# Optimization experiments

Hardware: AMD Instinct MI355X
Metric: run time of the kernel (lower is better)

## Reference

```python
import jax, jax.numpy as jnp
import numpy as np

MARGIN = 0.3
N, D = 4096, 512
NUM_CLASSES = 64

def setup_inputs() -> dict:
    key = jax.random.key(0)
    k1, k2, k3 = jax.random.split(key, 3)
    src_feat = jax.random.normal(k1, (N, D), dtype=jnp.float32)
    tgt_feat = jax.random.normal(k2, (N, D), dtype=jnp.float32)
    labels = jax.random.randint(k3, (N,), 0, NUM_CLASSES, dtype=jnp.int64)
    return {"src_feat": src_feat, "tgt_feat": tgt_feat, "labels": labels}

def reference(src_feat, tgt_feat, labels):
    # squared Euclidean distance matrix [n, n]
    e1 = jnp.sum(src_feat * src_feat, axis=1, keepdims=True)   # [n,1]
    e2 = jnp.sum(tgt_feat * tgt_feat, axis=1, keepdims=True).T  # [1,n]
    dist = e1 + e2 - 2.0 * (src_feat @ tgt_feat.T)
    dist = jnp.maximum(dist, 0.0)  # matches dist_mat[dist_mat < 0] = 0
    # same-label mask [n, n]
    mask = labels[:, None] == labels[None, :]
    # hard positive: max dist among same-label cols; hard negative: min among others
    dist_ap = jnp.max(jnp.where(mask, dist, -jnp.inf), axis=1)  # [n]
    dist_an = jnp.min(jnp.where(mask, jnp.inf, dist), axis=1)   # [n]
    # MarginRankingLoss with target y = 1: mean(relu(-(an - ap) + margin))
    loss = jnp.mean(jax.nn.relu(dist_ap - dist_an + MARGIN))
    return loss
```

## Files before the change

kernel.cpp:

```cpp
#include <hip/hip_runtime.h>
#include <hip/hip_bf16.h>
#include <stdint.h>

#define N_PTS 4096
#define DIM 512
#define MARGIN_F 0.3f
#define POS_INF_BITS 0x7f800000

typedef short bf16x8 __attribute__((ext_vector_type(8)));
typedef float f32x4 __attribute__((ext_vector_type(4)));

__device__ __forceinline__ unsigned short f2bf(float f) {
    unsigned int b = __float_as_uint(f);
    b += 0x7FFF + ((b >> 16) & 1);
    return (unsigned short)(b >> 16);
}

__device__ __forceinline__ void async16(const unsigned short* g, unsigned short* l) {
    __builtin_amdgcn_global_load_lds(
        (const __attribute__((address_space(1))) unsigned int*)g,
        (__attribute__((address_space(3))) unsigned int*)l,
        16, 0, 0);
}

#define RAW_BARRIER()  asm volatile("s_barrier" ::: "memory")
#define WAIT_VM12()    asm volatile("s_waitcnt vmcnt(12)" ::: "memory")
#define WAIT_VM6()     asm volatile("s_waitcnt vmcnt(6)" ::: "memory")
#define WAIT_VM0()     asm volatile("s_waitcnt vmcnt(0)" ::: "memory")

__global__ __launch_bounds__(256) void prep_kernel(
    const float* __restrict__ src, const float* __restrict__ tgt,
    unsigned short* __restrict__ src_bf, unsigned short* __restrict__ tgt_bf,
    float* __restrict__ e1, float* __restrict__ e2,
    float* __restrict__ out)
{
    const int row  = blockIdx.x * 4 + (threadIdx.x >> 6);
    const int lane = threadIdx.x & 63;

    if (blockIdx.x == 0 && threadIdx.x == 0) out[0] = 0.0f;

    const float4* s4 = (const float4*)(src + (size_t)row * DIM);
    const float4* t4 = (const float4*)(tgt + (size_t)row * DIM);
    float4 a0 = s4[lane], a1 = s4[lane + 64];
    float4 b0 = t4[lane], b1 = t4[lane + 64];

    ushort4 u;
    ushort4* so = (ushort4*)(src_bf + (size_t)row * DIM);
    ushort4* to = (ushort4*)(tgt_bf + (size_t)row * DIM);
    u.x = f2bf(a0.x); u.y = f2bf(a0.y); u.z = f2bf(a0.z); u.w = f2bf(a0.w); so[lane] = u;
    u.x = f2bf(a1.x); u.y = f2bf(a1.y); u.z = f2bf(a1.z); u.w = f2bf(a1.w); so[lane + 64] = u;
    u.x = f2bf(b0.x); u.y = f2bf(b0.y); u.z = f2bf(b0.z); u.w = f2bf(b0.w); to[lane] = u;
    u.x = f2bf(b1.x); u.y = f2bf(b1.y); u.z = f2bf(b1.z); u.w = f2bf(b1.w); to[lane + 64] = u;

    float s1 = a0.x*a0.x + a0.y*a0.y + a0.z*a0.z + a0.w*a0.w
             + a1.x*a1.x + a1.y*a1.y + a1.z*a1.z + a1.w*a1.w;
    float s2 = b0.x*b0.x + b0.y*b0.y + b0.z*b0.z + b0.w*b0.w
             + b1.x*b1.x + b1.y*b1.y + b1.z*b1.z + b1.w*b1.w;
    for (int off = 32; off; off >>= 1) {
        s1 += __shfl_down(s1, off);
        s2 += __shfl_down(s2, off);
    }
    if (lane == 0) {
        e1[row] = s1;
        e2[row] = s2;
    }
}

#define BM 128
#define BN 256
#define BK 32
#define NSTEP (DIM / BK)
#define NPART 64

__global__ __launch_bounds__(256, 2) void dist_kernel(
    const unsigned short* __restrict__ src_bf,
    const unsigned short* __restrict__ tgt_bf,
    const float* __restrict__ e1, const float* __restrict__ e2,
    const int* __restrict__ labels,
    float* __restrict__ ap_part, float* __restrict__ an_part)
{
    __shared__ unsigned short As[3][BM * BK];
    __shared__ unsigned short Bs[3][BN * BK];
    __shared__ int   li[BM];
    __shared__ int   lj[BN];
    __shared__ float e1s[BM];
    __shared__ float e2s[BN];

    const int i0 = blockIdx.y * BM;
    const int j0 = blockIdx.x * BN;
    const int t = threadIdx.x;
    const int lane = t & 63;
    const int wave = t >> 6;

    lj[t] = labels[j0 + t];
    e2s[t] = e2[j0 + t];
    if (t < BM) { li[t] = labels[i0 + t]; e1s[t] = e1[i0 + t]; }

    const int srow = t >> 2;
    const int scol = ((t & 3) ^ ((srow >> 1) & 3)) * 8;
    const unsigned short* gA0 = src_bf + (size_t)(i0 + srow) * DIM + scol;
    const unsigned short* gA1 = src_bf + (size_t)(i0 + 64 + srow) * DIM + scol;
    const unsigned short* gB0 = tgt_bf + (size_t)(j0 + srow) * DIM + scol;
    const unsigned short* gB1 = tgt_bf + (size_t)(j0 + 64 + srow) * DIM + scol;
    const unsigned short* gB2 = tgt_bf + (size_t)(j0 + 128 + srow) * DIM + scol;
    const unsigned short* gB3 = tgt_bf + (size_t)(j0 + 192 + srow) * DIM + scol;
    const int aOff0 = wave * 512;
    const int aOff1 = 2048 + wave * 512;
    const int bOff0 = wave * 512;
    const int bOff1 = 2048 + wave * 512;
    const int bOff2 = 4096 + wave * 512;
    const int bOff3 = 6144 + wave * 512;

    const int wn = wave * 64;
    const int fr = lane & 15;
    const int quad = lane >> 4;
    const int fkey = (fr >> 1) & 3;
    const int cp = (quad ^ fkey) * 8;

    f32x4 acc[8][4];
    #pragma unroll
    for (int a = 0; a < 8; a++)
        #pragma unroll
        for (int b = 0; b < 4; b++)
            acc[a][b] = (f32x4){0.f, 0.f, 0.f, 0.f};

    #pragma unroll
    for (int p = 0; p < 2; p++) {
        const int kk = p * BK;
        async16(gA0 + kk, &As[p][0] + aOff0);
        async16(gA1 + kk, &As[p][0] + aOff1);
        async16(gB0 + kk, &Bs[p][0] + bOff0);
        async16(gB1 + kk, &Bs[p][0] + bOff1);
        async16(gB2 + kk, &Bs[p][0] + bOff2);
        async16(gB3 + kk, &Bs[p][0] + bOff3);
    }

    #pragma unroll
    for (int s = 0; s < NSTEP; s++) {
        if (s + 2 < NSTEP) {
            const int kk = (s + 2) * BK;
            const int nb = (s + 2) % 3;
            async16(gA0 + kk, &As[nb][0] + aOff0);
            async16(gA1 + kk, &As[nb][0] + aOff1);
            async16(gB0 + kk, &Bs[nb][0] + bOff0);
            async16(gB1 + kk, &Bs[nb][0] + bOff1);
            async16(gB2 + kk, &Bs[nb][0] + bOff2);
            async16(gB3 + kk, &Bs[nb][0] + bOff3);
            WAIT_VM12();
        } else if (s + 2 == NSTEP) {
            WAIT_VM6();
        } else {
            WAIT_VM0();
        }
        RAW_BARRIER();

        const unsigned short* aa = &As[s % 3][0];
        const unsigned short* bb = &Bs[s % 3][0];
        bf16x8 af[8], bf[4];
        #pragma unroll
        for (int x = 0; x < 8; x++)
            af[x] = *(const bf16x8*)&aa[(x * 16 + fr) * BK + cp];
        #pragma unroll
        for (int x = 0; x < 4; x++)
            bf[x] = *(const bf16x8*)&bb[(wn + x * 16 + fr) * BK + cp];
        #pragma unroll
        for (int tm = 0; tm < 8; tm++)
            #pragma unroll
            for (int tn = 0; tn < 4; tn++)
                acc[tm][tn] = __builtin_amdgcn_mfma_f32_16x16x32_bf16(
                    af[tm], bf[tn], acc[tm][tn], 0, 0, 0);

        if (s + 1 < NSTEP)
            RAW_BARRIER();
    }

    const float INF = __int_as_float(POS_INF_BITS);
    const int pcol = blockIdx.x * 4 + wave;
    #pragma unroll
    for (int tm = 0; tm < 8; tm++) {
        #pragma unroll
        for (int r = 0; r < 4; r++) {
            const int rl = tm * 16 + quad * 4 + r;
            const float e1v = e1s[rl];
            const int   liv = li[rl];
            float apv = 0.0f;
            float anv = INF;
            #pragma unroll
            for (int tn = 0; tn < 4; tn++) {
                const int cl = wn + tn * 16 + fr;
                float d = e1v + e2s[cl] - 2.0f * acc[tm][tn][r];
                d = fmaxf(d, 0.0f);
                if (liv == lj[cl]) apv = fmaxf(apv, d);
                else               anv = fminf(anv, d);
            }
            #pragma unroll
            for (int off = 1; off < 16; off <<= 1) {
                apv = fmaxf(apv, __shfl_xor(apv, off));
                anv = fminf(anv, __shfl_xor(anv, off));
            }
            if (fr == 0) {
                ap_part[(size_t)(i0 + rl) * NPART + pcol] = apv;
                an_part[(size_t)(i0 + rl) * NPART + pcol] = anv;
            }
        }
    }
}

__global__ __launch_bounds__(128) void loss_kernel(
    const float* __restrict__ ap_part, const float* __restrict__ an_part,
    float* __restrict__ out)
{
    const int row = blockIdx.x * 128 + threadIdx.x;
    const float4* a4 = (const float4*)(ap_part + (size_t)row * NPART);
    const float4* n4 = (const float4*)(an_part + (size_t)row * NPART);
    float apv = 0.0f;
    float anv = __int_as_float(POS_INF_BITS);
    #pragma unroll
    for (int i = 0; i < NPART / 4; i++) {
        float4 a = a4[i], n = n4[i];
        apv = fmaxf(apv, fmaxf(fmaxf(a.x, a.y), fmaxf(a.z, a.w)));
        anv = fminf(anv, fminf(fminf(n.x, n.y), fminf(n.z, n.w)));
    }
    float s = fmaxf(apv - anv + MARGIN_F, 0.0f);
    for (int off = 32; off; off >>= 1) s += __shfl_down(s, off);
    __shared__ float red[2];
    if ((threadIdx.x & 63) == 0) red[threadIdx.x >> 6] = s;
    __syncthreads();
    if (threadIdx.x == 0)
        atomicAdd(out, (red[0] + red[1]) / (float)N_PTS);
}

extern "C" void kernel_launch(void* const* d_in, const int* in_sizes, int n_in,
                              void* d_out, int out_size, void* d_ws, size_t ws_size,
                              hipStream_t stream) {
    const float* src   = (const float*)d_in[0];
    const float* tgt   = (const float*)d_in[1];
    const int* labels  = (const int*)d_in[2];

    char* ws = (char*)d_ws;
    const size_t featB = (size_t)N_PTS * DIM * sizeof(unsigned short);
    unsigned short* src_bf = (unsigned short*)ws;
    unsigned short* tgt_bf = (unsigned short*)(ws + featB);
    float* e1 = (float*)(ws + 2 * featB);
    float* e2 = e1 + N_PTS;
    float* ap_part = e2 + N_PTS;
    float* an_part = ap_part + (size_t)N_PTS * NPART;

    prep_kernel<<<N_PTS / 4, 256, 0, stream>>>(src, tgt, src_bf, tgt_bf,
                                               e1, e2, (float*)d_out);
    dim3 grid(N_PTS / BN, N_PTS / BM);
    dist_kernel<<<grid, 256, 0, stream>>>(src_bf, tgt_bf, e1, e2, labels,
                                          ap_part, an_part);
    loss_kernel<<<N_PTS / 128, 128, 0, stream>>>(ap_part, an_part, (float*)d_out);
}
```

Baseline: 101.4 us.

## Shrink distance tile to 128x128 with 2x2 waves and double buffering

Halves the block's N tile from 256 to 128 and arranges the four waves as a 2x2 grid of 64x64 sub-tiles. The LDS pipeline drops from triple to double buffering, with the next prefetch issued after the MFMA phase. The kernel now requests 4 blocks per CU and launches twice as many blocks, which aims at better occupancy and load balance across CUs. In exchange, each tile reuses its loaded operands less per flop and the prefetch pipeline is shallower, so load latency may be less well hidden.

```diff
diff --git a/kernel.cpp b/kernel.cpp
--- a/kernel.cpp
+++ b/kernel.cpp
@@ -24,8 +24,7 @@
 }
 
 #define RAW_BARRIER()  asm volatile("s_barrier" ::: "memory")
-#define WAIT_VM12()    asm volatile("s_waitcnt vmcnt(12)" ::: "memory")
-#define WAIT_VM6()     asm volatile("s_waitcnt vmcnt(6)" ::: "memory")
+#define WAIT_VM4()     asm volatile("s_waitcnt vmcnt(4)" ::: "memory")
 #define WAIT_VM0()     asm volatile("s_waitcnt vmcnt(0)" ::: "memory")
 
 __global__ __launch_bounds__(256) void prep_kernel(
@@ -67,20 +66,20 @@
 }
 
 #define BM 128
-#define BN 256
+#define BN 128
 #define BK 32
 #define NSTEP (DIM / BK)
 #define NPART 64
 
-__global__ __launch_bounds__(256, 2) void dist_kernel(
+__global__ __launch_bounds__(256, 4) void dist_kernel(
     const unsigned short* __restrict__ src_bf,
     const unsigned short* __restrict__ tgt_bf,
     const float* __restrict__ e1, const float* __restrict__ e2,
     const int* __restrict__ labels,
     float* __restrict__ ap_part, float* __restrict__ an_part)
 {
-    __shared__ unsigned short As[3][BM * BK];
-    __shared__ unsigned short Bs[3][BN * BK];
+    __shared__ unsigned short As[2][BM * BK];
+    __shared__ unsigned short Bs[2][BN * BK];
     __shared__ int   li[BM];
     __shared__ int   lj[BN];
     __shared__ float e1s[BM];
@@ -92,34 +91,32 @@
     const int lane = t & 63;
     const int wave = t >> 6;
 
-    lj[t] = labels[j0 + t];
-    e2s[t] = e2[j0 + t];
-    if (t < BM) { li[t] = labels[i0 + t]; e1s[t] = e1[i0 + t]; }
+    if (t < BM) {
+        li[t]  = labels[i0 + t];
+        e1s[t] = e1[i0 + t];
+        lj[t]  = labels[j0 + t];
+        e2s[t] = e2[j0 + t];
+    }
 
     const int srow = t >> 2;
     const int scol = ((t & 3) ^ ((srow >> 1) & 3)) * 8;
     const unsigned short* gA0 = src_bf + (size_t)(i0 + srow) * DIM + scol;
-    const unsigned short* gA1 = src_bf + (size_t)(i0 + 64 + srow) * DIM + scol;
+    const unsigned short* gA1 = gA0 + (size_t)64 * DIM;
     const unsigned short* gB0 = tgt_bf + (size_t)(j0 + srow) * DIM + scol;
-    const unsigned short* gB1 = tgt_bf + (size_t)(j0 + 64 + srow) * DIM + scol;
-    const unsigned short* gB2 = tgt_bf + (size_t)(j0 + 128 + srow) * DIM + scol;
-    const unsigned short* gB3 = tgt_bf + (size_t)(j0 + 192 + srow) * DIM + scol;
-    const int aOff0 = wave * 512;
-    const int aOff1 = 2048 + wave * 512;
-    const int bOff0 = wave * 512;
-    const int bOff1 = 2048 + wave * 512;
-    const int bOff2 = 4096 + wave * 512;
-    const int bOff3 = 6144 + wave * 512;
-
-    const int wn = wave * 64;
+    const unsigned short* gB1 = gB0 + (size_t)64 * DIM;
+    const int off0 = wave * 512;
+    const int off1 = 2048 + wave * 512;
+
+    const int wm = (wave >> 1) * 64;
+    const int wn = (wave & 1) * 64;
     const int fr = lane & 15;
     const int quad = lane >> 4;
     const int fkey = (fr >> 1) & 3;
     const int cp = (quad ^ fkey) * 8;
 
-    f32x4 acc[8][4];
-    #pragma unroll
-    for (int a = 0; a < 8; a++)
+    f32x4 acc[4][4];
+    #pragma unroll
+    for (int a = 0; a < 4; a++)
         #pragma unroll
         for (int b = 0; b < 4; b++)
             acc[a][b] = (f32x4){0.f, 0.f, 0.f, 0.f};
@@ -127,60 +124,52 @@
     #pragma unroll
     for (int p = 0; p < 2; p++) {
         const int kk = p * BK;
-        async16(gA0 + kk, &As[p][0] + aOff0);
-        async16(gA1 + kk, &As[p][0] + aOff1);
-        async16(gB0 + kk, &Bs[p][0] + bOff0);
-        async16(gB1 + kk, &Bs[p][0] + bOff1);
-        async16(gB2 + kk, &Bs[p][0] + bOff2);
-        async16(gB3 + kk, &Bs[p][0] + bOff3);
+        async16(gA0 + kk, &As[p][0] + off0);
+        async16(gA1 + kk, &As[p][0] + off1);
+        async16(gB0 + kk, &Bs[p][0] + off0);
+        async16(gB1 + kk, &Bs[p][0] + off1);
     }
 
     #pragma unroll
     for (int s = 0; s < NSTEP; s++) {
-        if (s + 2 < NSTEP) {
-            const int kk = (s + 2) * BK;
-            const int nb = (s + 2) % 3;
-            async16(gA0 + kk, &As[nb][0] + aOff0);
-            async16(gA1 + kk, &As[nb][0] + aOff1);
-            async16(gB0 + kk, &Bs[nb][0] + bOff0);
-            async16(gB1 + kk, &Bs[nb][0] + bOff1);
-            async16(gB2 + kk, &Bs[nb][0] + bOff2);
-            async16(gB3 + kk, &Bs[nb][0] + bOff3);
-            WAIT_VM12();
-        } else if (s + 2 == NSTEP) {
-            WAIT_VM6();
-        } else {
-            WAIT_VM0();
-        }
+        if (s == NSTEP - 1) WAIT_VM0();
+        else                WAIT_VM4();
         RAW_BARRIER();
 
-        const unsigned short* aa = &As[s % 3][0];
-        const unsigned short* bb = &Bs[s % 3][0];
-        bf16x8 af[8], bf[4];
-        #pragma unroll
-        for (int x = 0; x < 8; x++)
-            af[x] = *(const bf16x8*)&aa[(x * 16 + fr) * BK + cp];
+        const unsigned short* aa = &As[s & 1][0];
+        const unsigned short* bb = &Bs[s & 1][0];
+        bf16x8 af[4], bfv[4];
         #pragma unroll
         for (int x = 0; x < 4; x++)
-            bf[x] = *(const bf16x8*)&bb[(wn + x * 16 + fr) * BK + cp];
-        #pragma unroll
-        for (int tm = 0; tm < 8; tm++)
+            af[x] = *(const bf16x8*)&aa[(wm + x * 16 + fr) * BK + cp];
+        #pragma unroll
+        for (int x = 0; x < 4; x++)
+            bfv[x] = *(const bf16x8*)&bb[(wn + x * 16 + fr) * BK + cp];
+        #pragma unroll
+        for (int tm = 0; tm < 4; tm++)
             #pragma unroll
             for (int tn = 0; tn < 4; tn++)
                 acc[tm][tn] = __builtin_amdgcn_mfma_f32_16x16x32_bf16(
-                    af[tm], bf[tn], acc[tm][tn], 0, 0, 0);
-
-        if (s + 1 < NSTEP)
+                    af[tm], bfv[tn], acc[tm][tn], 0, 0, 0);
+
+        if (s + 2 < NSTEP) {
             RAW_BARRIER();
+            const int kk = (s + 2) * BK;
+            const int nb = s & 1;
+            async16(gA0 + kk, &As[nb][0] + off0);
+            async16(gA1 + kk, &As[nb][0] + off1);
+            async16(gB0 + kk, &Bs[nb][0] + off0);
+            async16(gB1 + kk, &Bs[nb][0] + off1);
+        }
     }
 
     const float INF = __int_as_float(POS_INF_BITS);
-    const int pcol = blockIdx.x * 4 + wave;
-    #pragma unroll
-    for (int tm = 0; tm < 8; tm++) {
+    const int pcol = blockIdx.x * 2 + (wave & 1);
+    #pragma unroll
+    for (int tm = 0; tm < 4; tm++) {
         #pragma unroll
         for (int r = 0; r < 4; r++) {
-            const int rl = tm * 16 + quad * 4 + r;
+            const int rl = wm + tm * 16 + quad * 4 + r;
             const float e1v = e1s[rl];
             const int   liv = li[rl];
             float apv = 0.0f;
```

Result: no change. 101.4 us (+0.0%).
